# Kernel optimization log

Hardware: AMD Instinct MI355X
Metric: run time of the kernel (lower is better)

The kernel has to match this reference:

```python
import jax, jax.numpy as jnp
import numpy as np

D_MODEL = 1024
D_FF = 4096
N_EXPERTS = 8
TOP_K = 2
B, S = 4, 2048


def setup_inputs() -> dict:
    key = jax.random.key(0)
    ks = jax.random.split(key, 6)
    x = jax.random.normal(ks[0], (B, S, D_MODEL), dtype=jnp.float32)
    # router gate: nn.Linear(d_model, num_experts, bias=False), weight [E, D]
    gate_w = jax.random.normal(ks[1], (N_EXPERTS, D_MODEL), dtype=jnp.float32) * 0.01
    # expert MLPs, xavier-uniform init
    lim1 = float(np.sqrt(6.0 / (D_MODEL + D_FF)))
    W1 = jax.random.uniform(ks[2], (N_EXPERTS, D_FF, D_MODEL), minval=-lim1, maxval=lim1, dtype=jnp.float32)
    b1 = jnp.zeros((N_EXPERTS, D_FF), dtype=jnp.float32)
    W2 = jax.random.uniform(ks[3], (N_EXPERTS, D_MODEL, D_FF), minval=-lim1, maxval=lim1, dtype=jnp.float32)
    b2 = jnp.zeros((N_EXPERTS, D_MODEL), dtype=jnp.float32)
    return {"x": x, "gate_w": gate_w, "W1": W1, "b1": b1, "W2": W2, "b2": b2}


def reference(x, gate_w, W1, b1, W2, b2):
    Bb, Ss, D = x.shape
    xt = x.reshape(-1, D)                                  # [N, D]
    # --- router ---
    logits = xt @ gate_w.T                                 # [N, E]
    probs = jax.nn.softmax(logits, axis=-1)
    w_topk, idx = jax.lax.top_k(probs, TOP_K)              # [N, K]
    w_topk = w_topk / (jnp.sum(w_topk, axis=-1, keepdims=True) + 1e-9)
    # dense combine weights: zero for unselected experts    [N, E]
    comb = jnp.sum(jax.nn.one_hot(idx, N_EXPERTS, dtype=xt.dtype) * w_topk[..., None], axis=1)
    # --- experts (dense grouped GEMM over all experts) ---
    h = jnp.einsum('nd,efd->enf', xt, W1) + b1[:, None, :]  # [E, N, ff]
    h = jax.nn.relu(h)                                      # dropout=identity (eval)
    y = jnp.einsum('enf,edf->end', h, W2) + b2[:, None, :]  # [E, N, D]
    # --- weighted scatter/combine ---
    out = jnp.einsum('ne,end->nd', comb, y)                 # [N, D]
    return out.reshape(Bb, Ss, D)
```

## Files before the change

### kernel.cpp

```cpp
#include <hip/hip_runtime.h>
#include <hip/hip_bf16.h>
#include <stdint.h>

#define D_MODEL 1024
#define D_FF    4096
#define N_EXP   8
#define TOPK    2
#define NTOK    8192
#define NASSIGN (NTOK*TOPK)

#define BM 128
#define BN 128
#define BK 64
#define THREADS 256

typedef __bf16 bf16_t;
typedef __attribute__((ext_vector_type(8))) bf16_t bf16x8;
typedef __attribute__((ext_vector_type(4))) float f32x4;
typedef __attribute__((ext_vector_type(4))) float f32v4;
typedef __attribute__((ext_vector_type(8))) unsigned short u16x8;
typedef __attribute__((ext_vector_type(4))) unsigned short u16x4;

__device__ __forceinline__ unsigned short f2bf(float f) {
    bf16_t b = (bf16_t)f;
    return __builtin_bit_cast(unsigned short, b);
}

__device__ __forceinline__ void gload_lds16(const void* g, void* l) {
    __builtin_amdgcn_global_load_lds(
        (const __attribute__((address_space(1))) void*)g,
        (__attribute__((address_space(3))) void*)l, 16, 0, 0);
}

__global__ __launch_bounds__(256) void fused_pre_kernel(
        const float* __restrict__ x, const float* __restrict__ gw,
        int* __restrict__ recE, float* __restrict__ recW,
        unsigned short* __restrict__ xb, float* __restrict__ out,
        const float* __restrict__ W1, unsigned short* __restrict__ o1, long n1,
        const float* __restrict__ W2, unsigned short* __restrict__ o2, long n2) {
    int blk = blockIdx.x;
    if (blk < 2048) {
        int w = threadIdx.x >> 6;
        int lane = threadIdx.x & 63;
        int n = blk * 4 + w;
        const float* xr = x + (size_t)n * D_MODEL;
        unsigned short* xbr = xb + (size_t)n * D_MODEL;
        float4 z = make_float4(0.f, 0.f, 0.f, 0.f);
        float4* orow4 = (float4*)(out + (size_t)n * D_MODEL);
        #pragma unroll
        for (int i = 0; i < 4; i++) orow4[lane + i * 64] = z;

        float acc[N_EXP];
        #pragma unroll
        for (int e = 0; e < N_EXP; e++) acc[e] = 0.f;
        #pragma unroll
        for (int i = 0; i < 4; i++) {
            int j = lane + i * 64;
            float4 v = ((const float4*)xr)[j];
            ushort4 o;
            o.x = f2bf(v.x); o.y = f2bf(v.y); o.z = f2bf(v.z); o.w = f2bf(v.w);
            ((ushort4*)xbr)[j] = o;
            int d = j * 4;
            #pragma unroll
            for (int e = 0; e < N_EXP; e++) {
                const float* g = gw + e * D_MODEL + d;
                acc[e] += v.x * g[0] + v.y * g[1] + v.z * g[2] + v.w * g[3];
            }
        }
        #pragma unroll
        for (int e = 0; e < N_EXP; e++) {
            #pragma unroll
            for (int off = 32; off > 0; off >>= 1)
                acc[e] += __shfl_down(acc[e], off);
        }
        if (lane == 0) {
            float mx = acc[0];
            #pragma unroll
            for (int e = 1; e < N_EXP; e++) mx = fmaxf(mx, acc[e]);
            float p[N_EXP];
            float s = 0.f;
            #pragma unroll
            for (int e = 0; e < N_EXP; e++) { p[e] = expf(acc[e] - mx); s += p[e]; }
            float inv = 1.f / s;
            #pragma unroll
            for (int e = 0; e < N_EXP; e++) p[e] *= inv;
            int i0 = 0;
            #pragma unroll
            for (int e = 1; e < N_EXP; e++) if (p[e] > p[i0]) i0 = e;
            int i1 = (i0 == 0) ? 1 : 0;
            #pragma unroll
            for (int e = 0; e < N_EXP; e++) if (e != i0 && p[e] > p[i1]) i1 = e;
            float s2 = p[i0] + p[i1] + 1e-9f;
            recE[2 * n]     = i0;  recW[2 * n]     = p[i0] / s2;
            recE[2 * n + 1] = i1;  recW[2 * n + 1] = p[i1] / s2;
        }
    } else {
        long stride = 2048L * 256;
        long q1 = n1 / 8, q2 = n2 / 8;
        for (long i = (long)(blk - 2048) * 256 + threadIdx.x; i < q1 + q2; i += stride) {
            const f32v4* src; u16x4* dst; long k;
            if (i < q1) { src = (const f32v4*)W1; dst = (u16x4*)o1; k = i; }
            else        { src = (const f32v4*)W2; dst = (u16x4*)o2; k = i - q1; }
            f32v4 v0 = __builtin_nontemporal_load(src + 2 * k);
            f32v4 v1 = __builtin_nontemporal_load(src + 2 * k + 1);
            u16x4 a, b;
            a.x = f2bf(v0.x); a.y = f2bf(v0.y); a.z = f2bf(v0.z); a.w = f2bf(v0.w);
            b.x = f2bf(v1.x); b.y = f2bf(v1.y); b.z = f2bf(v1.z); b.w = f2bf(v1.w);
            __builtin_nontemporal_store(a, dst + 2 * k);
            __builtin_nontemporal_store(b, dst + 2 * k + 1);
        }
    }
}

__global__ __launch_bounds__(512) void build_lists_kernel(
        const int* __restrict__ recE, const float* __restrict__ recW,
        int* __restrict__ counts, int* __restrict__ offs,
        int* __restrict__ ltok, float* __restrict__ lw) {
    int we = threadIdx.x >> 6;
    int lane = threadIdx.x & 63;
    int base = 0;
    for (int j0 = 0; j0 < NASSIGN; j0 += 64) {
        int e = recE[j0 + lane];
        float wt = recW[j0 + lane];
        unsigned long long m = __ballot(e == we);
        if (e == we) {
            int pos = base + __builtin_popcountll(m & ((1ull << lane) - 1));
            ltok[we * NTOK + pos] = (j0 + lane) >> 1;
            lw[we * NTOK + pos] = wt;
        }
        base += __builtin_popcountll(m);
    }
    if (lane == 0) counts[we] = base;
    __syncthreads();
    if (threadIdx.x == 0) {
        int s = 0;
        for (int e = 0; e < N_EXP; e++) { offs[e] = s; s += counts[e]; }
    }
}

__global__ __launch_bounds__(THREADS, 3) void gemm1_kernel(
        const unsigned short* __restrict__ xb, const unsigned short* __restrict__ w1b,
        const float* __restrict__ b1,
        const int* __restrict__ counts, const int* __restrict__ offs,
        const int* __restrict__ ltok,
        unsigned short* __restrict__ hb) {
    const int NTM = NTOK / BM;
    int b = blockIdx.x;
    int e = b & 7;
    int idx = b >> 3;
    int nt = idx / NTM;
    int mt = idx % NTM;
    int cnt = counts[e];
    if (mt * BM >= cnt) return;

    __shared__ __align__(16) unsigned short As[BM * BK];
    __shared__ __align__(16) unsigned short Bs[BN * BK];

    int t = threadIdx.x;
    int lane = t & 63, w = t >> 6;
    int wr = w >> 1, wc = w & 1;

    int srow = t >> 3;
    int schunk = (t & 7) ^ (srow & 7);
    const unsigned short* aptr[4];
    const unsigned short* bptr[4];
    #pragma unroll
    for (int j = 0; j < 4; j++) {
        int rr = srow + j * 32;
        int slot = mt * BM + rr;
        int cs = slot < cnt ? slot : (cnt - 1);
        int tok = ltok[e * NTOK + cs];
        aptr[j] = xb + (size_t)tok * D_MODEL + schunk * 8;
        bptr[j] = w1b + ((size_t)e * D_FF + nt * BN + rr) * D_MODEL + schunk * 8;
    }
    char* As_b = (char*)As;
    char* Bs_b = (char*)Bs;

    int arow_base = wr * 64 + (lane & 15);
    int brow_base = wc * 64 + (lane & 15);
    int ch[2];
    #pragma unroll
    for (int ks = 0; ks < 2; ks++)
        ch[ks] = ((ks * 4 + (lane >> 4)) ^ (lane & 7)) << 4;

    f32x4 acc[4][4];
    #pragma unroll
    for (int m = 0; m < 4; m++)
        #pragma unroll
        for (int n = 0; n < 4; n++)
            acc[m][n] = (f32x4){0.f, 0.f, 0.f, 0.f};

    for (int k0 = 0; k0 < D_MODEL; k0 += BK) {
        #pragma unroll
        for (int j = 0; j < 4; j++) {
            gload_lds16(aptr[j] + k0, As_b + j * 4096 + t * 16);
            gload_lds16(bptr[j] + k0, Bs_b + j * 4096 + t * 16);
        }
        __syncthreads();
        bf16x8 af[2][4], bf[2][4];
        #pragma unroll
        for (int ks = 0; ks < 2; ks++) {
            #pragma unroll
            for (int m = 0; m < 4; m++)
                af[ks][m] = *(const bf16x8*)(As_b + (size_t)(arow_base + m * 16) * 128 + ch[ks]);
            #pragma unroll
            for (int n = 0; n < 4; n++)
                bf[ks][n] = *(const bf16x8*)(Bs_b + (size_t)(brow_base + n * 16) * 128 + ch[ks]);
        }
        #pragma unroll
        for (int ks = 0; ks < 2; ks++)
            #pragma unroll
            for (int m = 0; m < 4; m++)
                #pragma unroll
                for (int n = 0; n < 4; n++)
                    acc[m][n] = __builtin_amdgcn_mfma_f32_16x16x32_bf16(af[ks][m], bf[ks][n], acc[m][n], 0, 0, 0);
        __syncthreads();
    }

    int hbase = offs[e];
    float biasv[4];
    #pragma unroll
    for (int n = 0; n < 4; ++n)
        biasv[n] = b1[e * D_FF + nt * BN + wc * 64 + n * 16 + (lane & 15)];
    unsigned short* Hs = (unsigned short*)(As_b) + w * 1216;
    #pragma unroll
    for (int m = 0; m < 4; ++m) {
        #pragma unroll
        for (int n = 0; n < 4; ++n) {
            #pragma unroll
            for (int rq = 0; rq < 4; ++rq) {
                int lr = (lane >> 4) * 4 + rq;
                int lc = n * 16 + (lane & 15);
                float v = fmaxf(acc[m][n][rq] + biasv[n], 0.f);
                Hs[lr * 72 + lc] = f2bf(v);
            }
        }
        #pragma unroll
        for (int half = 0; half < 2; ++half) {
            int lr = half * 8 + (lane >> 3);
            u16x8 vv = *(const u16x8*)(Hs + lr * 72 + (lane & 7) * 8);
            int s = mt * BM + wr * 64 + m * 16 + lr;
            if (s < cnt) {
                *(u16x8*)(hb + (size_t)(hbase + s) * D_FF + nt * BN + wc * 64 + (lane & 7) * 8) = vv;
            }
        }
    }
}

__global__ __launch_bounds__(THREADS, 3) void gemm2_kernel(
        const unsigned short* __restrict__ hb, const unsigned short* __restrict__ w2b,
        const float* __restrict__ b2,
        const int* __restrict__ counts, const int* __restrict__ offs,
        const int* __restrict__ ltok, const float* __restrict__ lw,
        float* __restrict__ out) {
    const int NTM = NTOK / BM;
    int b = blockIdx.x;
    int e = b & 7;
    int idx = b >> 3;
    int nt = idx / NTM;
    int mt = idx % NTM;
    int cnt = counts[e];
    if (mt * BM >= cnt) return;
    int hbase = offs[e];

    __shared__ __align__(16) unsigned short As[BM * BK];
    __shared__ __align__(16) unsigned short Bs[BN * BK];

    int t = threadIdx.x;
    int lane = t & 63, w = t >> 6;
    int wr = w >> 1, wc = w & 1;

    int srow = t >> 3;
    int schunk = (t & 7) ^ (srow & 7);
    const unsigned short* aptr[4];
    const unsigned short* bptr[4];
    #pragma unroll
    for (int j = 0; j < 4; j++) {
        int rr = srow + j * 32;
        int slot = mt * BM + rr;
        int cs = slot < cnt ? slot : (cnt - 1);
        aptr[j] = hb + (size_t)(hbase + cs) * D_FF + schunk * 8;
        bptr[j] = w2b + ((size_t)e * D_MODEL + nt * BN + rr) * D_FF + schunk * 8;
    }
    char* As_b = (char*)As;
    char* Bs_b = (char*)Bs;

    int arow_base = wr * 64 + (lane & 15);
    int brow_base = wc * 64 + (lane & 15);
    int ch[2];
    #pragma unroll
    for (int ks = 0; ks < 2; ks++)
        ch[ks] = ((ks * 4 + (lane >> 4)) ^ (lane & 7)) << 4;

    f32x4 acc[4][4];
    #pragma unroll
    for (int m = 0; m < 4; m++)
        #pragma unroll
        for (int n = 0; n < 4; n++)
            acc[m][n] = (f32x4){0.f, 0.f, 0.f, 0.f};

    for (int k0 = 0; k0 < D_FF; k0 += BK) {
        #pragma unroll
        for (int j = 0; j < 4; j++) {
            gload_lds16(aptr[j] + k0, As_b + j * 4096 + t * 16);
            gload_lds16(bptr[j] + k0, Bs_b + j * 4096 + t * 16);
        }
        __syncthreads();
        bf16x8 af[2][4], bf[2][4];
        #pragma unroll
        for (int ks = 0; ks < 2; ks++) {
            #pragma unroll
            for (int m = 0; m < 4; m++)
                af[ks][m] = *(const bf16x8*)(As_b + (size_t)(arow_base + m * 16) * 128 + ch[ks]);
            #pragma unroll
            for (int n = 0; n < 4; n++)
                bf[ks][n] = *(const bf16x8*)(Bs_b + (size_t)(brow_base + n * 16) * 128 + ch[ks]);
        }
        #pragma unroll
        for (int ks = 0; ks < 2; ks++)
            #pragma unroll
            for (int m = 0; m < 4; m++)
                #pragma unroll
                for (int n = 0; n < 4; n++)
                    acc[m][n] = __builtin_amdgcn_mfma_f32_16x16x32_bf16(af[ks][m], bf[ks][n], acc[m][n], 0, 0, 0);
        __syncthreads();
    }

    int lbase = e * NTOK;
    float biasv[4];
    #pragma unroll
    for (int n = 0; n < 4; ++n)
        biasv[n] = b2[e * D_MODEL + nt * BN + wc * 64 + n * 16 + (lane & 15)];
    #pragma unroll
    for (int m = 0; m < 4; ++m) {
        int s0 = mt * BM + wr * 64 + m * 16 + (lane >> 4) * 4;
        #pragma unroll
        for (int rq = 0; rq < 4; ++rq) {
            int s = s0 + rq;
            if (s >= cnt) continue;
            int tok = ltok[lbase + s];
            float wgt = lw[lbase + s];
            float* orow = out + (size_t)tok * D_MODEL + nt * BN + wc * 64 + (lane & 15);
            #pragma unroll
            for (int n = 0; n < 4; ++n)
                atomicAdd(orow + n * 16, wgt * (acc[m][n][rq] + biasv[n]));
        }
    }
}

extern "C" void kernel_launch(void* const* d_in, const int* in_sizes, int n_in,
                              void* d_out, int out_size, void* d_ws, size_t ws_size,
                              hipStream_t stream) {
    const float* x  = (const float*)d_in[0];
    const float* gw = (const float*)d_in[1];
    const float* W1 = (const float*)d_in[2];
    const float* b1 = (const float*)d_in[3];
    const float* W2 = (const float*)d_in[4];
    const float* b2 = (const float*)d_in[5];
    float* out = (float*)d_out;

    char* ws = (char*)d_ws;
    size_t off = 0;
    auto alloc = [&](size_t bytes) -> char* {
        char* p = ws + off;
        off += (bytes + 255) & ~(size_t)255;
        return p;
    };
    unsigned short* xb  = (unsigned short*)alloc((size_t)NTOK * D_MODEL * 2);
    unsigned short* w1b = (unsigned short*)alloc((size_t)N_EXP * D_FF * D_MODEL * 2);
    unsigned short* w2b = (unsigned short*)alloc((size_t)N_EXP * D_MODEL * D_FF * 2);
    unsigned short* hb  = (unsigned short*)alloc((size_t)NASSIGN * D_FF * 2);
    int*   counts = (int*)alloc(256);
    int*   offs   = (int*)alloc(256);
    int*   ltok   = (int*)alloc((size_t)N_EXP * NTOK * 4);
    float* lw     = (float*)alloc((size_t)N_EXP * NTOK * 4);
    int*   recE   = (int*)alloc((size_t)NASSIGN * 4);
    float* recW   = (float*)alloc((size_t)NASSIGN * 4);

    fused_pre_kernel<<<4096, 256, 0, stream>>>(
        x, gw, recE, recW, xb, out,
        W1, w1b, (long)N_EXP * D_FF * D_MODEL, W2, w2b, (long)N_EXP * D_MODEL * D_FF);
    build_lists_kernel<<<1, 512, 0, stream>>>(recE, recW, counts, offs, ltok, lw);
    gemm1_kernel<<<N_EXP * (NTOK / BM) * (D_FF / BN), THREADS, 0, stream>>>(
        xb, w1b, b1, counts, offs, ltok, hb);
    gemm2_kernel<<<N_EXP * (NTOK / BM) * (D_MODEL / BN), THREADS, 0, stream>>>(
        hb, w2b, b2, counts, offs, ltok, lw, out);
}
```

Measured before the change: 599.2 us.

## Move W2 bf16 conversion into gemm1 launch to overlap with expert GEMM

The fp32-to-bf16 conversion of W2 is taken out of the pre-processing kernel and handed to extra blocks appended to the gemm1 grid, which only reads W1. This lets the memory-bound W2 conversion run alongside the compute-bound first GEMM instead of before it. The risk is that the conversion blocks are scheduled after most GEMM blocks, since they have the highest block indices, so little overlap may happen. They also compete with the GEMM for bandwidth and CU slots.

```diff
diff --git a/kernel.cpp b/kernel.cpp
--- a/kernel.cpp
+++ b/kernel.cpp
@@ -13,6 +13,8 @@
 #define BN 128
 #define BK 64
 #define THREADS 256
+#define G1_BLOCKS (N_EXP * (NTOK / BM) * (D_FF / BN))
+#define CVT_BLOCKS 2048
 
 typedef __bf16 bf16_t;
 typedef __attribute__((ext_vector_type(8))) bf16_t bf16x8;
@@ -32,12 +34,29 @@
         (__attribute__((address_space(3))) void*)l, 16, 0, 0);
 }
 
+__device__ __forceinline__ void cvt_stream(const float* __restrict__ W,
+                                           unsigned short* __restrict__ o,
+                                           long n, long blk0) {
+    long stride = (long)CVT_BLOCKS * 256;
+    long q = n / 8;
+    for (long i = blk0 * 256 + threadIdx.x; i < q; i += stride) {
+        const f32v4* src = (const f32v4*)W;
+        u16x4* dst = (u16x4*)o;
+        f32v4 v0 = __builtin_nontemporal_load(src + 2 * i);
+        f32v4 v1 = __builtin_nontemporal_load(src + 2 * i + 1);
+        u16x4 a, b;
+        a.x = f2bf(v0.x); a.y = f2bf(v0.y); a.z = f2bf(v0.z); a.w = f2bf(v0.w);
+        b.x = f2bf(v1.x); b.y = f2bf(v1.y); b.z = f2bf(v1.z); b.w = f2bf(v1.w);
+        __builtin_nontemporal_store(a, dst + 2 * i);
+        __builtin_nontemporal_store(b, dst + 2 * i + 1);
+    }
+}
+
 __global__ __launch_bounds__(256) void fused_pre_kernel(
         const float* __restrict__ x, const float* __restrict__ gw,
         int* __restrict__ recE, float* __restrict__ recW,
         unsigned short* __restrict__ xb, float* __restrict__ out,
-        const float* __restrict__ W1, unsigned short* __restrict__ o1, long n1,
-        const float* __restrict__ W2, unsigned short* __restrict__ o2, long n2) {
+        const float* __restrict__ W1, unsigned short* __restrict__ o1, long n1) {
     int blk = blockIdx.x;
     if (blk < 2048) {
         int w = threadIdx.x >> 6;
@@ -95,20 +114,7 @@
             recE[2 * n + 1] = i1;  recW[2 * n + 1] = p[i1] / s2;
         }
     } else {
-        long stride = 2048L * 256;
-        long q1 = n1 / 8, q2 = n2 / 8;
-        for (long i = (long)(blk - 2048) * 256 + threadIdx.x; i < q1 + q2; i += stride) {
-            const f32v4* src; u16x4* dst; long k;
-            if (i < q1) { src = (const f32v4*)W1; dst = (u16x4*)o1; k = i; }
-            else        { src = (const f32v4*)W2; dst = (u16x4*)o2; k = i - q1; }
-            f32v4 v0 = __builtin_nontemporal_load(src + 2 * k);
-            f32v4 v1 = __builtin_nontemporal_load(src + 2 * k + 1);
-            u16x4 a, b;
-            a.x = f2bf(v0.x); a.y = f2bf(v0.y); a.z = f2bf(v0.z); a.w = f2bf(v0.w);
-            b.x = f2bf(v1.x); b.y = f2bf(v1.y); b.z = f2bf(v1.z); b.w = f2bf(v1.w);
-            __builtin_nontemporal_store(a, dst + 2 * k);
-            __builtin_nontemporal_store(b, dst + 2 * k + 1);
-        }
+        cvt_stream(W1, o1, n1, blk - 2048);
     }
 }
 
@@ -143,9 +149,14 @@
         const float* __restrict__ b1,
         const int* __restrict__ counts, const int* __restrict__ offs,
         const int* __restrict__ ltok,
-        unsigned short* __restrict__ hb) {
+        unsigned short* __restrict__ hb,
+        const float* __restrict__ W2, unsigned short* __restrict__ o2, long n2) {
     const int NTM = NTOK / BM;
     int b = blockIdx.x;
+    if (b >= G1_BLOCKS) {
+        cvt_stream(W2, o2, n2, b - G1_BLOCKS);
+        return;
+    }
     int e = b & 7;
     int idx = b >> 3;
     int nt = idx / NTM;
@@ -378,11 +389,11 @@
     float* recW   = (float*)alloc((size_t)NASSIGN * 4);
 
     fused_pre_kernel<<<4096, 256, 0, stream>>>(
-        x, gw, recE, recW, xb, out,
-        W1, w1b, (long)N_EXP * D_FF * D_MODEL, W2, w2b, (long)N_EXP * D_MODEL * D_FF);
+        x, gw, recE, recW, xb, out, W1, w1b, (long)N_EXP * D_FF * D_MODEL);
     build_lists_kernel<<<1, 512, 0, stream>>>(recE, recW, counts, offs, ltok, lw);
-    gemm1_kernel<<<N_EXP * (NTOK / BM) * (D_FF / BN), THREADS, 0, stream>>>(
-        xb, w1b, b1, counts, offs, ltok, hb);
+    gemm1_kernel<<<G1_BLOCKS + CVT_BLOCKS, THREADS, 0, stream>>>(
+        xb, w1b, b1, counts, offs, ltok, hb,
+        W2, w2b, (long)N_EXP * D_MODEL * D_FF);
     gemm2_kernel<<<N_EXP * (NTOK / BM) * (D_MODEL / BN), THREADS, 0, stream>>>(
         hb, w2b, b2, counts, offs, ltok, lw, out);
 }
```

Result: no change. 590.5 us (-1.5%).
